# Performance work log

Hardware: AMD Instinct MI355X
Metric: run time of the kernel (lower is better)

The kernel has to match this reference:

```python
import jax, jax.numpy as jnp
import numpy as np

N, M, P, D = 64, 64, 256, 64
EPS = 1e-8


def setup_inputs() -> dict:
    key = jax.random.key(0)
    k1, k2 = jax.random.split(key)
    normal_embed = jax.random.normal(k1, (N, P, D), dtype=jnp.float32)
    defect_embed = jax.random.normal(k2, (M, P, D), dtype=jnp.float32)
    return {"normal_embed": normal_embed, "defect_embed": defect_embed}


def _normalize(x):
    # x / (||x|| + eps) along last dim, matching torch .norm(dim=-1, keepdim=True)
    return x / (jnp.linalg.norm(x, axis=-1, keepdims=True) + EPS)


def _patch_similarities(a, b):
    # a: [N,P,D] normalized, b: [M,Q,D] normalized -> [N,M]
    # replaces the torch double Python loop with one batched einsum
    s = jnp.einsum("npd,mqd->nmpq", a, b)  # pairwise patch cosine sims
    return s.max(axis=3).mean(axis=2)       # max over b-patches, mean over a-patches


def reference(normal_embed, defect_embed):
    n = _normalize(normal_embed)
    d = _normalize(defect_embed)

    nn_sim = _patch_similarities(n, n)  # [N,N]
    nd_sim = _patch_similarities(n, d)  # [N,M]

    nN = nn_sim.shape[0]
    off_mask = ~jnp.eye(nN, dtype=bool)
    cnt = nN * (nN - 1)  # number of off-diagonal entries (static)

    mu_nn = jnp.sum(jnp.where(off_mask, nn_sim, 0.0)) / cnt
    # unbiased std (torch default, ddof=1) over off-diagonal entries
    var_nn = jnp.sum(jnp.where(off_mask, (nn_sim - mu_nn) ** 2, 0.0)) / (cnt - 1)
    sigma_nn = jnp.sqrt(var_nn)

    mu_nd = jnp.mean(nd_sim)
    sigma_nd = jnp.std(nd_sim, ddof=1)

    separability = (mu_nn - mu_nd) / (sigma_nn + sigma_nd + EPS)
    loss = -separability
    return loss
```

## Files before the change

### kernel.cpp

```cpp
#include <hip/hip_runtime.h>
#include <math.h>

#define EPS 1e-8f

typedef __attribute__((ext_vector_type(8))) short bf16x8;
typedef __attribute__((ext_vector_type(4))) float f32x4;

__device__ __forceinline__ unsigned short f2bf(float f) {
    unsigned int u = __float_as_uint(f);
    unsigned int r = (u + 0x7fffu + ((u >> 16) & 1u)) >> 16;
    return (unsigned short)r;
}
__device__ __forceinline__ float bf2f(unsigned short h) {
    return __uint_as_float(((unsigned int)h) << 16);
}

__global__ __launch_bounds__(256) void prep_kernel(
    const float* __restrict__ normal, const float* __restrict__ defect,
    unsigned short* __restrict__ fragN_hi, unsigned short* __restrict__ fragN_lo,
    unsigned short* __restrict__ fragD_hi, unsigned short* __restrict__ fragD_lo)
{
    const int gimg = blockIdx.x;
    const bool isN = gimg < 64;
    const int img  = isN ? gimg : gimg - 64;
    const float* src = isN ? normal : defect;
    unsigned short* dhi = isN ? fragN_hi : fragD_hi;
    unsigned short* dlo = isN ? fragN_lo : fragD_lo;

    const int patch = threadIdx.x;
    const float4* xp = (const float4*)(src + ((size_t)img * 256 + patch) * 64);
    float x[64];
    float ss = 0.f;
    #pragma unroll
    for (int k = 0; k < 16; ++k) {
        float4 v = xp[k];
        x[4*k+0] = v.x; x[4*k+1] = v.y; x[4*k+2] = v.z; x[4*k+3] = v.w;
        ss += v.x*v.x + v.y*v.y + v.z*v.z + v.w*v.w;
    }
    const float inv = 1.f / (sqrtf(ss) + EPS);

    const int t  = patch >> 4;
    const int ll = patch & 15;
    #pragma unroll
    for (int s = 0; s < 2; ++s) {
        #pragma unroll
        for (int g = 0; g < 4; ++g) {
            const size_t off = ((((size_t)img * 16 + t) * 2 + s) * 64 + (g * 16 + ll)) * 8;
            unsigned short h8[8], l8[8];
            #pragma unroll
            for (int e = 0; e < 8; ++e) {
                const float v = x[s*32 + g*8 + e] * inv;
                const unsigned short hb = f2bf(v);
                h8[e] = hb;
                l8[e] = f2bf(v - bf2f(hb));
            }
            *(uint4*)(dhi + off) = *(const uint4*)h8;
            *(uint4*)(dlo + off) = *(const uint4*)l8;
        }
    }
}

__global__ __launch_bounds__(256) void mfma_sim_kernel(
    const unsigned short* __restrict__ fragN_hi, const unsigned short* __restrict__ fragN_lo,
    const unsigned short* __restrict__ fragD_hi, const unsigned short* __restrict__ fragD_lo,
    float* __restrict__ sim)
{
    const int t = threadIdx.x;
    const int l = t & 63;
    const int w = t >> 6;
    const int b = blockIdx.x;

    int i, j;
    bool is_nd;
    if (b < 4096) {
        is_nd = true;
        i = b >> 6;
        j = b & 63;
    } else {
        is_nd = false;
        int kk = b - 4096;
        int ii = 0;
        while (kk >= 63 - ii) { kk -= 63 - ii; ++ii; }
        i = ii;
        j = ii + 1 + kk;
    }
    const unsigned short* bhi_base = is_nd ? fragD_hi : fragN_hi;
    const unsigned short* blo_base = is_nd ? fragD_lo : fragN_lo;

    __shared__ float cp[16][4][16];
    __shared__ float wpart[4];
    __shared__ float csum[4];

    bf16x8 ah[4][2], al[4][2];
    #pragma unroll
    for (int r = 0; r < 4; ++r) {
        #pragma unroll
        for (int s = 0; s < 2; ++s) {
            const size_t off = ((((size_t)i * 16 + (w*4 + r)) * 2 + s) * 64 + l) * 8;
            ah[r][s] = *(const bf16x8*)(fragN_hi + off);
            al[r][s] = *(const bf16x8*)(fragN_lo + off);
        }
    }

    f32x4 rowmax[4];
    #pragma unroll
    for (int r = 0; r < 4; ++r)
        rowmax[r] = (f32x4){-3e38f, -3e38f, -3e38f, -3e38f};

    const size_t jb = (size_t)j * 16;

    #define COMPUTE_TILE(CT, BH, BL) do {                                        \
        f32x4 m4 = (f32x4){-3e38f, -3e38f, -3e38f, -3e38f};                      \
        _Pragma("unroll")                                                        \
        for (int r = 0; r < 4; ++r) {                                            \
            f32x4 acc = (f32x4){0.f, 0.f, 0.f, 0.f};                             \
            __builtin_amdgcn_s_setprio(1);                                       \
            _Pragma("unroll")                                                    \
            for (int s = 0; s < 2; ++s) {                                        \
                acc = __builtin_amdgcn_mfma_f32_16x16x32_bf16(al[r][s], BH[s], acc, 0, 0, 0); \
                acc = __builtin_amdgcn_mfma_f32_16x16x32_bf16(ah[r][s], BL[s], acc, 0, 0, 0); \
                acc = __builtin_amdgcn_mfma_f32_16x16x32_bf16(ah[r][s], BH[s], acc, 0, 0, 0); \
            }                                                                    \
            __builtin_amdgcn_s_setprio(0);                                       \
            _Pragma("unroll")                                                    \
            for (int e = 0; e < 4; ++e) {                                        \
                rowmax[r][e] = fmaxf(rowmax[r][e], acc[e]);                      \
                m4[e] = fmaxf(m4[e], acc[e]);                                    \
            }                                                                    \
        }                                                                        \
        if (!is_nd) {                                                            \
            float cmv = fmaxf(fmaxf(m4[0], m4[1]), fmaxf(m4[2], m4[3]));         \
            cmv = fmaxf(cmv, __shfl_xor(cmv, 16));                               \
            cmv = fmaxf(cmv, __shfl_xor(cmv, 32));                               \
            if (l < 16) cp[CT][w][l] = cmv;                                      \
        }                                                                        \
    } while (0)

    bf16x8 bh0[2], bl0[2], bh1[2], bl1[2];
    #pragma unroll
    for (int s = 0; s < 2; ++s) {
        const size_t off = (((jb + 0) * 2 + s) * 64 + l) * 8;
        bh0[s] = *(const bf16x8*)(bhi_base + off);
        bl0[s] = *(const bf16x8*)(blo_base + off);
    }

    #pragma unroll 1
    for (int c = 0; c < 16; c += 2) {
        #pragma unroll
        for (int s = 0; s < 2; ++s) {
            const size_t off = (((jb + c + 1) * 2 + s) * 64 + l) * 8;
            bh1[s] = *(const bf16x8*)(bhi_base + off);
            bl1[s] = *(const bf16x8*)(blo_base + off);
        }
        COMPUTE_TILE(c, bh0, bl0);
        if (c < 14) {
            #pragma unroll
            for (int s = 0; s < 2; ++s) {
                const size_t off = (((jb + c + 2) * 2 + s) * 64 + l) * 8;
                bh0[s] = *(const bf16x8*)(bhi_base + off);
                bl0[s] = *(const bf16x8*)(blo_base + off);
            }
        }
        COMPUTE_TILE(c + 1, bh1, bl1);
    }
    #undef COMPUTE_TILE

    float s_sum = 0.f;
    #pragma unroll
    for (int r = 0; r < 4; ++r) {
        #pragma unroll
        for (int e = 0; e < 4; ++e) {
            float v = rowmax[r][e];
            v = fmaxf(v, __shfl_xor(v, 1));
            v = fmaxf(v, __shfl_xor(v, 2));
            v = fmaxf(v, __shfl_xor(v, 4));
            v = fmaxf(v, __shfl_xor(v, 8));
            s_sum += v;
        }
    }
    #pragma unroll
    for (int off = 1; off < 64; off <<= 1)
        s_sum += __shfl_xor(s_sum, off);

    if (l == 0) wpart[w] = s_sum;
    __syncthreads();
    if (t == 0) {
        const float sim_v = (wpart[0] + wpart[1] + wpart[2] + wpart[3]) * (1.f / (16.f * 256.f));
        sim[(is_nd ? 4096 : 0) + i * 64 + j] = sim_v;
    }

    if (!is_nd) {
        const int ct = t >> 4;
        const int cl = t & 15;
        float m = fmaxf(fmaxf(cp[ct][0][cl], cp[ct][1][cl]),
                        fmaxf(cp[ct][2][cl], cp[ct][3][cl]));
        #pragma unroll
        for (int off = 1; off < 64; off <<= 1)
            m += __shfl_xor(m, off);
        if (l == 0) csum[w] = m;
        __syncthreads();
        if (t == 0) {
            const float sim_v = (csum[0] + csum[1] + csum[2] + csum[3]) * (1.f / 256.f);
            sim[j * 64 + i] = sim_v;
        }
    }
}

__global__ __launch_bounds__(256) void sim_kernel_f32(
    const float* __restrict__ normal, const float* __restrict__ defect,
    float* __restrict__ sim)
{
    __shared__ float Bs[256 * 64];
    const int t = threadIdx.x;
    const int pair = blockIdx.x;
    const int i = pair >> 7;
    const int j2 = pair & 127;
    const bool is_nn = (j2 < 64);
    const int j = is_nn ? j2 : (j2 - 64);
    const float* bsrc = is_nn ? normal : defect;

    {
        const float4* bp = (const float4*)(bsrc + ((size_t)j * 256 + t) * 64);
        float4 bv[16];
        float ss = 0.f;
        #pragma unroll
        for (int k = 0; k < 16; ++k) {
            bv[k] = bp[k];
            ss += bv[k].x*bv[k].x + bv[k].y*bv[k].y + bv[k].z*bv[k].z + bv[k].w*bv[k].w;
        }
        const float inv = 1.f / (sqrtf(ss) + EPS);
        float4* bq = (float4*)&Bs[t * 64];
        #pragma unroll
        for (int k = 0; k < 16; ++k) {
            float4 v = bv[k];
            v.x *= inv; v.y *= inv; v.z *= inv; v.w *= inv;
            bq[k] = v;
        }
    }
    float a[64];
    {
        const float4* ap = (const float4*)(normal + ((size_t)i * 256 + t) * 64);
        float ss = 0.f;
        #pragma unroll
        for (int k = 0; k < 16; ++k) {
            float4 v = ap[k];
            a[4*k+0] = v.x; a[4*k+1] = v.y; a[4*k+2] = v.z; a[4*k+3] = v.w;
            ss += v.x*v.x + v.y*v.y + v.z*v.z + v.w*v.w;
        }
        const float inv = 1.f / (sqrtf(ss) + EPS);
        #pragma unroll
        for (int d = 0; d < 64; ++d) a[d] *= inv;
    }
    __syncthreads();
    float maxv = -1e30f;
    #pragma unroll 2
    for (int q = 0; q < 256; ++q) {
        const float4* bq = (const float4*)&Bs[q * 64];
        float acc0 = 0.f, acc1 = 0.f;
        #pragma unroll
        for (int k = 0; k < 8; ++k) {
            float4 b0 = bq[k];
            float4 b1 = bq[k + 8];
            acc0 += a[4*k+0]*b0.x + a[4*k+1]*b0.y + a[4*k+2]*b0.z + a[4*k+3]*b0.w;
            acc1 += a[4*(k+8)+0]*b1.x + a[4*(k+8)+1]*b1.y + a[4*(k+8)+2]*b1.z + a[4*(k+8)+3]*b1.w;
        }
        maxv = fmaxf(maxv, acc0 + acc1);
    }
    __syncthreads();
    float s = maxv;
    #pragma unroll
    for (int off = 32; off > 0; off >>= 1) s += __shfl_down(s, off);
    const int wid = t >> 6;
    if ((t & 63) == 0) Bs[wid] = s;
    __syncthreads();
    if (t == 0) {
        const float sim_v = (Bs[0] + Bs[1] + Bs[2] + Bs[3]) * (1.f / 256.f);
        sim[(is_nn ? 0 : 4096) + i * 64 + j] = sim_v;
    }
}

__global__ __launch_bounds__(256) void stats_kernel(const float* __restrict__ sim,
                                                    float* __restrict__ out)
{
    const int t = threadIdx.x;
    double snn = 0, qnn = 0, snd = 0, qnd = 0;
    for (int k = t; k < 4096; k += 256) {
        const int r = k >> 6, c = k & 63;
        const float vnn = sim[k];
        if (r != c) { snn += vnn; qnn += (double)vnn * vnn; }
        const float vnd = sim[4096 + k];
        snd += vnd; qnd += (double)vnd * vnd;
    }
    #pragma unroll
    for (int off = 32; off > 0; off >>= 1) {
        snn += __shfl_down(snn, off);
        qnn += __shfl_down(qnn, off);
        snd += __shfl_down(snd, off);
        qnd += __shfl_down(qnd, off);
    }
    __shared__ double red[4][4];
    const int wid = t >> 6;
    if ((t & 63) == 0) { red[0][wid] = snn; red[1][wid] = qnn; red[2][wid] = snd; red[3][wid] = qnd; }
    __syncthreads();
    if (t == 0) {
        const double SN = red[0][0] + red[0][1] + red[0][2] + red[0][3];
        const double QN = red[1][0] + red[1][1] + red[1][2] + red[1][3];
        const double SD = red[2][0] + red[2][1] + red[2][2] + red[2][3];
        const double QD = red[3][0] + red[3][1] + red[3][2] + red[3][3];
        const double cnt = 64.0 * 63.0;
        const double mu_nn = SN / cnt;
        double var_nn = (QN - cnt * mu_nn * mu_nn) / (cnt - 1.0);
        if (var_nn < 0) var_nn = 0;
        const double sig_nn = sqrt(var_nn);
        const double mu_nd = SD / 4096.0;
        double var_nd = (QD - 4096.0 * mu_nd * mu_nd) / 4095.0;
        if (var_nd < 0) var_nd = 0;
        const double sig_nd = sqrt(var_nd);
        const double sep = (mu_nn - mu_nd) / (sig_nn + sig_nd + 1e-8);
        out[0] = (float)(-sep);
    }
}

extern "C" void kernel_launch(void* const* d_in, const int* in_sizes, int n_in,
                              void* d_out, int out_size, void* d_ws, size_t ws_size,
                              hipStream_t stream) {
    const float* normal = (const float*)d_in[0];
    const float* defect = (const float*)d_in[1];
    float* out = (float*)d_out;

    const size_t FRAG = (size_t)64 * 16 * 2 * 64 * 8;
    const size_t need = FRAG * 4 * sizeof(unsigned short) + 8192 * sizeof(float);

    if (ws_size >= need) {
        unsigned short* base = (unsigned short*)d_ws;
        unsigned short* fNh = base;
        unsigned short* fNl = base + FRAG;
        unsigned short* fDh = base + 2 * FRAG;
        unsigned short* fDl = base + 3 * FRAG;
        float* sim = (float*)(base + 4 * FRAG);

        prep_kernel<<<128, 256, 0, stream>>>(normal, defect, fNh, fNl, fDh, fDl);
        mfma_sim_kernel<<<4096 + 2016, 256, 0, stream>>>(fNh, fNl, fDh, fDl, sim);
        stats_kernel<<<1, 256, 0, stream>>>(sim, out);
    } else {
        float* sim = (float*)d_ws;
        sim_kernel_f32<<<8192, 256, 0, stream>>>(normal, defect, sim);
        stats_kernel<<<1, 256, 0, stream>>>(sim, out);
    }
}
```

Baseline: 135.2 us.

## Process four defect images per block to reuse loaded normal fragments

The normal-vs-defect blocks now each handle four defect images for one normal image, so the A-operand fragments are loaded once per four pairs rather than once per pair. This cuts the grid from 4096+2016 blocks to 1024+2016 and splits the kernel into separate nd and nn branches, removing the runtime is_nd checks. In exchange there are fewer, longer blocks with more serial work each, which may reduce latency hiding and load balance across CUs.

```diff
diff --git a/kernel.cpp b/kernel.cpp
--- a/kernel.cpp
+++ b/kernel.cpp
@@ -70,126 +70,213 @@
     const int w = t >> 6;
     const int b = blockIdx.x;
 
-    int i, j;
-    bool is_nd;
-    if (b < 4096) {
-        is_nd = true;
-        i = b >> 6;
-        j = b & 63;
+    __shared__ float cp[16][4][16];
+    __shared__ float wj[4][4];
+    __shared__ float wpart[4];
+    __shared__ float csum[4];
+
+    if (b < 1024) {
+        const int i  = b >> 4;
+        const int j0 = (b & 15) * 4;
+
+        bf16x8 ah[4][2], al[4][2];
+        #pragma unroll
+        for (int r = 0; r < 4; ++r) {
+            #pragma unroll
+            for (int s = 0; s < 2; ++s) {
+                const size_t off = ((((size_t)i * 16 + (w*4 + r)) * 2 + s) * 64 + l) * 8;
+                ah[r][s] = *(const bf16x8*)(fragN_hi + off);
+                al[r][s] = *(const bf16x8*)(fragN_lo + off);
+            }
+        }
+
+        #define COMPUTE_ND(BH, BL) do {                                          \
+            _Pragma("unroll")                                                    \
+            for (int r = 0; r < 4; ++r) {                                        \
+                f32x4 acc = (f32x4){0.f, 0.f, 0.f, 0.f};                         \
+                __builtin_amdgcn_s_setprio(1);                                   \
+                _Pragma("unroll")                                                \
+                for (int s = 0; s < 2; ++s) {                                    \
+                    acc = __builtin_amdgcn_mfma_f32_16x16x32_bf16(al[r][s], BH[s], acc, 0, 0, 0); \
+                    acc = __builtin_amdgcn_mfma_f32_16x16x32_bf16(ah[r][s], BL[s], acc, 0, 0, 0); \
+                    acc = __builtin_amdgcn_mfma_f32_16x16x32_bf16(ah[r][s], BH[s], acc, 0, 0, 0); \
+                }                                                                \
+                __builtin_amdgcn_s_setprio(0);                                   \
+                _Pragma("unroll")                                                \
+                for (int e = 0; e < 4; ++e)                                      \
+                    rowmax[r][e] = fmaxf(rowmax[r][e], acc[e]);                  \
+            }                                                                    \
+        } while (0)
+
+        #pragma unroll 1
+        for (int jj = 0; jj < 4; ++jj) {
+            const size_t jb = (size_t)(j0 + jj) * 16;
+
+            f32x4 rowmax[4];
+            #pragma unroll
+            for (int r = 0; r < 4; ++r)
+                rowmax[r] = (f32x4){-3e38f, -3e38f, -3e38f, -3e38f};
+
+            bf16x8 bh0[2], bl0[2], bh1[2], bl1[2];
+            #pragma unroll
+            for (int s = 0; s < 2; ++s) {
+                const size_t off = (((jb + 0) * 2 + s) * 64 + l) * 8;
+                bh0[s] = *(const bf16x8*)(fragD_hi + off);
+                bl0[s] = *(const bf16x8*)(fragD_lo + off);
+            }
+
+            #pragma unroll 1
+            for (int c = 0; c < 16; c += 2) {
+                #pragma unroll
+                for (int s = 0; s < 2; ++s) {
+                    const size_t off = (((jb + c + 1) * 2 + s) * 64 + l) * 8;
+                    bh1[s] = *(const bf16x8*)(fragD_hi + off);
+                    bl1[s] = *(const bf16x8*)(fragD_lo + off);
+                }
+                COMPUTE_ND(bh0, bl0);
+                if (c < 14) {
+                    #pragma unroll
+                    for (int s = 0; s < 2; ++s) {
+                        const size_t off = (((jb + c + 2) * 2 + s) * 64 + l) * 8;
+                        bh0[s] = *(const bf16x8*)(fragD_hi + off);
+                        bl0[s] = *(const bf16x8*)(fragD_lo + off);
+                    }
+                }
+                COMPUTE_ND(bh1, bl1);
+            }
+
+            float s_sum = 0.f;
+            #pragma unroll
+            for (int r = 0; r < 4; ++r) {
+                #pragma unroll
+                for (int e = 0; e < 4; ++e) {
+                    float v = rowmax[r][e];
+                    v = fmaxf(v, __shfl_xor(v, 1));
+                    v = fmaxf(v, __shfl_xor(v, 2));
+                    v = fmaxf(v, __shfl_xor(v, 4));
+                    v = fmaxf(v, __shfl_xor(v, 8));
+                    s_sum += v;
+                }
+            }
+            #pragma unroll
+            for (int off = 1; off < 64; off <<= 1)
+                s_sum += __shfl_xor(s_sum, off);
+            if (l == 0) wj[w][jj] = s_sum;
+        }
+        #undef COMPUTE_ND
+
+        __syncthreads();
+        if (t < 4) {
+            const float sim_v = (wj[0][t] + wj[1][t] + wj[2][t] + wj[3][t])
+                                * (1.f / (16.f * 256.f));
+            sim[4096 + i * 64 + (j0 + t)] = sim_v;
+        }
     } else {
-        is_nd = false;
-        int kk = b - 4096;
+        int kk = b - 1024;
         int ii = 0;
         while (kk >= 63 - ii) { kk -= 63 - ii; ++ii; }
-        i = ii;
-        j = ii + 1 + kk;
-    }
-    const unsigned short* bhi_base = is_nd ? fragD_hi : fragN_hi;
-    const unsigned short* blo_base = is_nd ? fragD_lo : fragN_lo;
-
-    __shared__ float cp[16][4][16];
-    __shared__ float wpart[4];
-    __shared__ float csum[4];
-
-    bf16x8 ah[4][2], al[4][2];
-    #pragma unroll
-    for (int r = 0; r < 4; ++r) {
+        const int i = ii;
+        const int j = ii + 1 + kk;
+
+        bf16x8 ah[4][2], al[4][2];
+        #pragma unroll
+        for (int r = 0; r < 4; ++r) {
+            #pragma unroll
+            for (int s = 0; s < 2; ++s) {
+                const size_t off = ((((size_t)i * 16 + (w*4 + r)) * 2 + s) * 64 + l) * 8;
+                ah[r][s] = *(const bf16x8*)(fragN_hi + off);
+                al[r][s] = *(const bf16x8*)(fragN_lo + off);
+            }
+        }
+
+        f32x4 rowmax[4];
+        #pragma unroll
+        for (int r = 0; r < 4; ++r)
+            rowmax[r] = (f32x4){-3e38f, -3e38f, -3e38f, -3e38f};
+
+        const size_t jb = (size_t)j * 16;
+
+        #define COMPUTE_NN(CT, BH, BL) do {                                      \
+            f32x4 m4 = (f32x4){-3e38f, -3e38f, -3e38f, -3e38f};                  \
+            _Pragma("unroll")                                                    \
+            for (int r = 0; r < 4; ++r) {                                        \
+                f32x4 acc = (f32x4){0.f, 0.f, 0.f, 0.f};                         \
+                __builtin_amdgcn_s_setprio(1);                                   \
+                _Pragma("unroll")                                                \
+                for (int s = 0; s < 2; ++s) {                                    \
+                    acc = __builtin_amdgcn_mfma_f32_16x16x32_bf16(al[r][s], BH[s], acc, 0, 0, 0); \
+                    acc = __builtin_amdgcn_mfma_f32_16x16x32_bf16(ah[r][s], BL[s], acc, 0, 0, 0); \
+                    acc = __builtin_amdgcn_mfma_f32_16x16x32_bf16(ah[r][s], BH[s], acc, 0, 0, 0); \
+                }                                                                \
+                __builtin_amdgcn_s_setprio(0);                                   \
+                _Pragma("unroll")                                                \
+                for (int e = 0; e < 4; ++e) {                                    \
+                    rowmax[r][e] = fmaxf(rowmax[r][e], acc[e]);                  \
+                    m4[e] = fmaxf(m4[e], acc[e]);                                \
+                }                                                                \
+            }                                                                    \
+            {                                                                    \
+                float cmv = fmaxf(fmaxf(m4[0], m4[1]), fmaxf(m4[2], m4[3]));     \
+                cmv = fmaxf(cmv, __shfl_xor(cmv, 16));                           \
+                cmv = fmaxf(cmv, __shfl_xor(cmv, 32));                           \
+                if (l < 16) cp[CT][w][l] = cmv;                                  \
+            }                                                                    \
+        } while (0)
+
+        bf16x8 bh0[2], bl0[2], bh1[2], bl1[2];
         #pragma unroll
         for (int s = 0; s < 2; ++s) {
-            const size_t off = ((((size_t)i * 16 + (w*4 + r)) * 2 + s) * 64 + l) * 8;
-            ah[r][s] = *(const bf16x8*)(fragN_hi + off);
-            al[r][s] = *(const bf16x8*)(fragN_lo + off);
-        }
-    }
-
-    f32x4 rowmax[4];
-    #pragma unroll
-    for (int r = 0; r < 4; ++r)
-        rowmax[r] = (f32x4){-3e38f, -3e38f, -3e38f, -3e38f};
-
-    const size_t jb = (size_t)j * 16;
-
-    #define COMPUTE_TILE(CT, BH, BL) do {                                        \
-        f32x4 m4 = (f32x4){-3e38f, -3e38f, -3e38f, -3e38f};                      \
-        _Pragma("unroll")                                                        \
-        for (int r = 0; r < 4; ++r) {                                            \
-            f32x4 acc = (f32x4){0.f, 0.f, 0.f, 0.f};                             \
-            __builtin_amdgcn_s_setprio(1);                                       \
-            _Pragma("unroll")                                                    \
-            for (int s = 0; s < 2; ++s) {                                        \
-                acc = __builtin_amdgcn_mfma_f32_16x16x32_bf16(al[r][s], BH[s], acc, 0, 0, 0); \
-                acc = __builtin_amdgcn_mfma_f32_16x16x32_bf16(ah[r][s], BL[s], acc, 0, 0, 0); \
-                acc = __builtin_amdgcn_mfma_f32_16x16x32_bf16(ah[r][s], BH[s], acc, 0, 0, 0); \
-            }                                                                    \
-            __builtin_amdgcn_s_setprio(0);                                       \
-            _Pragma("unroll")                                                    \
-            for (int e = 0; e < 4; ++e) {                                        \
-                rowmax[r][e] = fmaxf(rowmax[r][e], acc[e]);                      \
-                m4[e] = fmaxf(m4[e], acc[e]);                                    \
-            }                                                                    \
-        }                                                                        \
-        if (!is_nd) {                                                            \
-            float cmv = fmaxf(fmaxf(m4[0], m4[1]), fmaxf(m4[2], m4[3]));         \
-            cmv = fmaxf(cmv, __shfl_xor(cmv, 16));                               \
-            cmv = fmaxf(cmv, __shfl_xor(cmv, 32));                               \
-            if (l < 16) cp[CT][w][l] = cmv;                                      \
-        }                                                                        \
-    } while (0)
-
-    bf16x8 bh0[2], bl0[2], bh1[2], bl1[2];
-    #pragma unroll
-    for (int s = 0; s < 2; ++s) {
-        const size_t off = (((jb + 0) * 2 + s) * 64 + l) * 8;
-        bh0[s] = *(const bf16x8*)(bhi_base + off);
-        bl0[s] = *(const bf16x8*)(blo_base + off);
-    }
-
-    #pragma unroll 1
-    for (int c = 0; c < 16; c += 2) {
-        #pragma unroll
-        for (int s = 0; s < 2; ++s) {
-            const size_t off = (((jb + c + 1) * 2 + s) * 64 + l) * 8;
-            bh1[s] = *(const bf16x8*)(bhi_base + off);
-            bl1[s] = *(const bf16x8*)(blo_base + off);
-        }
-        COMPUTE_TILE(c, bh0, bl0);
-        if (c < 14) {
+            const size_t off = (((jb + 0) * 2 + s) * 64 + l) * 8;
+            bh0[s] = *(const bf16x8*)(fragN_hi + off);
+            bl0[s] = *(const bf16x8*)(fragN_lo + off);
+        }
+
+        #pragma unroll 1
+        for (int c = 0; c < 16; c += 2) {
             #pragma unroll
             for (int s = 0; s < 2; ++s) {
-                const size_t off = (((jb + c + 2) * 2 + s) * 64 + l) * 8;
-                bh0[s] = *(const bf16x8*)(bhi_base + off);
-                bl0[s] = *(const bf16x8*)(blo_base + off);
-            }
-        }
-        COMPUTE_TILE(c + 1, bh1, bl1);
-    }
-    #undef COMPUTE_TILE
-
-    float s_sum = 0.f;
-    #pragma unroll
-    for (int r = 0; r < 4; ++r) {
-        #pragma unroll
-        for (int e = 0; e < 4; ++e) {
-            float v = rowmax[r][e];
-            v = fmaxf(v, __shfl_xor(v, 1));
-            v = fmaxf(v, __shfl_xor(v, 2));
-            v = fmaxf(v, __shfl_xor(v, 4));
-            v = fmaxf(v, __shfl_xor(v, 8));
-            s_sum += v;
-        }
-    }
-    #pragma unroll
-    for (int off = 1; off < 64; off <<= 1)
-        s_sum += __shfl_xor(s_sum, off);
-
-    if (l == 0) wpart[w] = s_sum;
-    __syncthreads();
-    if (t == 0) {
-        const float sim_v = (wpart[0] + wpart[1] + wpart[2] + wpart[3]) * (1.f / (16.f * 256.f));
-        sim[(is_nd ? 4096 : 0) + i * 64 + j] = sim_v;
-    }
-
-    if (!is_nd) {
+                const size_t off = (((jb + c + 1) * 2 + s) * 64 + l) * 8;
+                bh1[s] = *(const bf16x8*)(fragN_hi + off);
+                bl1[s] = *(const bf16x8*)(fragN_lo + off);
+            }
+            COMPUTE_NN(c, bh0, bl0);
+            if (c < 14) {
+                #pragma unroll
+                for (int s = 0; s < 2; ++s) {
+                    const size_t off = (((jb + c + 2) * 2 + s) * 64 + l) * 8;
+                    bh0[s] = *(const bf16x8*)(fragN_hi + off);
+                    bl0[s] = *(const bf16x8*)(fragN_lo + off);
+                }
+            }
+            COMPUTE_NN(c + 1, bh1, bl1);
+        }
+        #undef COMPUTE_NN
+
+        float s_sum = 0.f;
+        #pragma unroll
+        for (int r = 0; r < 4; ++r) {
+            #pragma unroll
+            for (int e = 0; e < 4; ++e) {
+                float v = rowmax[r][e];
+                v = fmaxf(v, __shfl_xor(v, 1));
+                v = fmaxf(v, __shfl_xor(v, 2));
+                v = fmaxf(v, __shfl_xor(v, 4));
+                v = fmaxf(v, __shfl_xor(v, 8));
+                s_sum += v;
+            }
+        }
+        #pragma unroll
+        for (int off = 1; off < 64; off <<= 1)
+            s_sum += __shfl_xor(s_sum, off);
+
+        if (l == 0) wpart[w] = s_sum;
+        __syncthreads();
+        if (t == 0) {
+            const float sim_v = (wpart[0] + wpart[1] + wpart[2] + wpart[3])
+                                * (1.f / (16.f * 256.f));
+            sim[i * 64 + j] = sim_v;
+        }
+
         const int ct = t >> 4;
         const int cl = t & 15;
         float m = fmaxf(fmaxf(cp[ct][0][cl], cp[ct][1][cl]),
@@ -340,7 +427,7 @@
         float* sim = (float*)(base + 4 * FRAG);
 
         prep_kernel<<<128, 256, 0, stream>>>(normal, defect, fNh, fNl, fDh, fDl);
-        mfma_sim_kernel<<<4096 + 2016, 256, 0, stream>>>(fNh, fNl, fDh, fDl, sim);
+        mfma_sim_kernel<<<1024 + 2016, 256, 0, stream>>>(fNh, fNl, fDh, fDl, sim);
         stats_kernel<<<1, 256, 0, stream>>>(sim, out);
     } else {
         float* sim = (float*)d_ws;
```

New measurement: 140.4 us. 3.9% more time.
